# Optimization experiments

Measured on AMD Instinct MI355X. Metric: run time of the kernel, lower is better.

The kernel has to match this reference:

```python
import jax, jax.numpy as jnp
import numpy as np

IMG_SIZE = 224  # matches init_kwargs img_size


def setup_inputs() -> dict:
    key = jax.random.key(0)
    k1, k2, k3 = jax.random.split(key, 3)
    B, N = 128, 16384
    points = jax.random.uniform(k1, (B, N, 3), dtype=jnp.float32, minval=-1.0, maxval=1.0)
    azimuth = jax.random.uniform(k2, (B,), dtype=jnp.float32, minval=0.0, maxval=2.0 * np.pi)
    elevation = jax.random.uniform(k3, (B,), dtype=jnp.float32, minval=-0.5, maxval=0.5)
    return {"points": points, "azimuth": azimuth, "elevation": elevation}


def _rotation_matrices(azimuth, elevation):
    cა, sა = jnp.cos(azimuth), jnp.sin(azimuth)
    ce, se = jnp.cos(elevation), jnp.sin(elevation)
    z = jnp.zeros_like(cა)
    o = jnp.ones_like(cა)
    # R_az: rotation about y-axis, shape (B,3,3)
    R_az = jnp.stack([
        jnp.stack([cა, z, sა], -1),
        jnp.stack([z, o, z], -1),
        jnp.stack([-sა, z, cა], -1),
    ], axis=-2)
    # R_el: rotation about x-axis
    R_el = jnp.stack([
        jnp.stack([o, z, z], -1),
        jnp.stack([z, ce, -se], -1),
        jnp.stack([z, se, ce], -1),
    ], axis=-2)
    return jnp.einsum('bij,bjk->bik', R_el, R_az)


def reference(points, azimuth, elevation):
    B, N, _ = points.shape
    H = W = IMG_SIZE
    R = _rotation_matrices(azimuth, elevation)                 # (B,3,3)
    rotated = jnp.einsum('bni,bji->bnj', points, R)            # points @ R^T -> (B,N,3)

    points_2d = rotated[..., :2]
    z = rotated[..., 2]
    z_min = jnp.min(z, axis=1, keepdims=True)
    z_max = jnp.max(z, axis=1, keepdims=True)
    feat = 0.3 + 0.7 * (z - z_min) / (z_max - z_min + 1e-6)    # (B,N)

    px = (points_2d[..., 0] + 1.0) * 0.5 * W - 0.5
    py = (points_2d[..., 1] + 1.0) * 0.5 * H - 0.5
    px1 = jnp.floor(px); py1 = jnp.floor(py)
    px2 = px1 + 1.0;     py2 = py1 + 1.0

    w11 = (px2 - px) * (py2 - py)
    w12 = (px2 - px) * (py - py1)
    w21 = (px - px1) * (py2 - py)
    w22 = (px - px1) * (py - py1)

    mask = (px1 >= 0) & (py1 >= 0) & (px2 < W) & (py2 < H)     # (B,N)
    # fuse mask + feature into the weights instead of compacting (jit-friendly)
    vals = jnp.stack([w11, w12, w21, w22], axis=-1)            # (B,N,4)
    vals = vals * (feat * mask.astype(feat.dtype))[..., None]

    px1i = jnp.clip(px1, 0, W - 1).astype(jnp.int32)
    py1i = jnp.clip(py1, 0, H - 1).astype(jnp.int32)
    px2i = jnp.clip(px2, 0, W - 1).astype(jnp.int32)
    py2i = jnp.clip(py2, 0, H - 1).astype(jnp.int32)
    base = (jnp.arange(B, dtype=jnp.int32) * (H * W))[:, None]  # (B,1)
    idx = jnp.stack([
        base + py1i * W + px1i,
        base + py2i * W + px1i,
        base + py1i * W + px2i,
        base + py2i * W + px2i,
    ], axis=-1)                                                 # (B,N,4)

    image = jnp.zeros(B * H * W, dtype=vals.dtype)
    image = image.at[idx.reshape(-1)].add(vals.reshape(-1))
    image = image.reshape(B, 1, H, W)
    return jnp.broadcast_to(image, (B, 3, H, W))
```

## Files before the change

kernel.cpp:

```cpp
#include <hip/hip_runtime.h>

#define IMG 224
#define HW (IMG * IMG)
#define HW4 (HW / 4)
#define NB 128
#define NPTS 16384

#define QUARTERS 4
#define RPB (IMG / QUARTERS)
#define TILE_FLOATS (RPB * IMG)
#define THREADS 512

__global__ __launch_bounds__(THREADS) void k_render(const float* __restrict__ pts,
                                                    const float* __restrict__ az,
                                                    const float* __restrict__ el,
                                                    float* __restrict__ out) {
    const int b = blockIdx.x & (NB - 1);
    const int q = blockIdx.x >> 7;
    const int y0 = q * RPB;

    __shared__ float tile[TILE_FLOATS];
    __shared__ float wmin[THREADS / 64], wmax[THREADS / 64];

    float sa, ca, se, ce;
    __sincosf(az[b], &sa, &ca);
    __sincosf(el[b], &se, &ce);
    const float r00 = ca,       r02 = sa;
    const float r10 = se * sa,  r11 = ce,  r12 = -se * ca;
    const float r20 = -ce * sa, r21 = se,  r22 = ce * ca;

    for (int i = threadIdx.x; i < TILE_FLOATS; i += THREADS) tile[i] = 0.0f;

    const float4* __restrict__ pb4 = (const float4*)(pts + (size_t)b * NPTS * 3);

    float zmin = 1e30f, zmax = -1e30f;
    for (int it = 0; it < NPTS / (4 * THREADS); ++it) {
        const int t = it * THREADS + threadIdx.x;
        const float4 v0 = pb4[3 * t + 0];
        const float4 v1 = pb4[3 * t + 1];
        const float4 v2 = pb4[3 * t + 2];
        float rz;
        rz = r20 * v0.x + r21 * v0.y + r22 * v0.z; zmin = fminf(zmin, rz); zmax = fmaxf(zmax, rz);
        rz = r20 * v0.w + r21 * v1.x + r22 * v1.y; zmin = fminf(zmin, rz); zmax = fmaxf(zmax, rz);
        rz = r20 * v1.z + r21 * v1.w + r22 * v2.x; zmin = fminf(zmin, rz); zmax = fmaxf(zmax, rz);
        rz = r20 * v2.y + r21 * v2.z + r22 * v2.w; zmin = fminf(zmin, rz); zmax = fmaxf(zmax, rz);
    }
    for (int m = 1; m < 64; m <<= 1) {
        zmin = fminf(zmin, __shfl_xor(zmin, m));
        zmax = fmaxf(zmax, __shfl_xor(zmax, m));
    }
    const int wid = threadIdx.x >> 6;
    if ((threadIdx.x & 63) == 0) { wmin[wid] = zmin; wmax[wid] = zmax; }
    __syncthreads();
    zmin = wmin[0]; zmax = wmax[0];
#pragma unroll
    for (int w = 1; w < THREADS / 64; ++w) {
        zmin = fminf(zmin, wmin[w]);
        zmax = fmaxf(zmax, wmax[w]);
    }
    const float inv = 0.7f / (zmax - zmin + 1e-6f);

    auto splat = [&](float x, float y, float z) {
        const float rx = r00 * x + r02 * z;
        const float ry = r10 * x + r11 * y + r12 * z;
        const float rz = r20 * x + r21 * y + r22 * z;
        const float feat = 0.3f + (rz - zmin) * inv;

        const float px = (rx + 1.0f) * (0.5f * IMG) - 0.5f;
        const float py = (ry + 1.0f) * (0.5f * IMG) - 0.5f;
        const float px1 = floorf(px);
        const float py1 = floorf(py);
        if (px1 >= 0.0f && py1 >= 0.0f && px1 < (float)(IMG - 1) && py1 < (float)(IMG - 1)) {
            const float wx2 = px - px1;
            const float wx1 = 1.0f - wx2;
            const float wy2 = py - py1;
            const float wy1 = 1.0f - wy2;

            const int ix = (int)px1;
            const int iy = (int)py1;
            const int r0 = iy - y0;
            const int r1 = r0 + 1;
            if (r0 >= 0 && r0 < RPB) {
                atomicAdd(&tile[r0 * IMG + ix],     wx1 * wy1 * feat);
                atomicAdd(&tile[r0 * IMG + ix + 1], wx2 * wy1 * feat);
            }
            if (r1 >= 0 && r1 < RPB) {
                atomicAdd(&tile[r1 * IMG + ix],     wx1 * wy2 * feat);
                atomicAdd(&tile[r1 * IMG + ix + 1], wx2 * wy2 * feat);
            }
        }
    };

    for (int it = 0; it < NPTS / (4 * THREADS); ++it) {
        const int t = it * THREADS + threadIdx.x;
        const float4 v0 = pb4[3 * t + 0];
        const float4 v1 = pb4[3 * t + 1];
        const float4 v2 = pb4[3 * t + 2];
        splat(v0.x, v0.y, v0.z);
        splat(v0.w, v1.x, v1.y);
        splat(v1.z, v1.w, v2.x);
        splat(v2.y, v2.z, v2.w);
    }

    __syncthreads();

    const float4* __restrict__ t4 = (const float4*)tile;
    float4* __restrict__ o4 = (float4*)(out + (size_t)b * 3 * HW + (size_t)y0 * IMG);
    for (int i = threadIdx.x; i < TILE_FLOATS / 4; i += THREADS) {
        const float4 v = t4[i];
        o4[i] = v;
        o4[i + HW4] = v;
        o4[i + 2 * HW4] = v;
    }
}

extern "C" void kernel_launch(void* const* d_in, const int* in_sizes, int n_in,
                              void* d_out, int out_size, void* d_ws, size_t ws_size,
                              hipStream_t stream) {
    const float* pts = (const float*)d_in[0];
    const float* az  = (const float*)d_in[1];
    const float* el  = (const float*)d_in[2];
    float* out = (float*)d_out;

    k_render<<<NB * QUARTERS, THREADS, 0, stream>>>(pts, az, el, out);
}
```

Measured before the change: 133.5 us.

## Split image into eight row bands, unroll loops, use nontemporal output stores

Each image is now split across 8 blocks of 28 rows instead of 4 blocks of 56 rows, giving twice as many blocks and a smaller shared tile. The price is that every block re-reads all points of its image and recomputes the z min/max. The point loops are fully unrolled, the feature computation moves inside the in-bounds branch, and the output is written with nontemporal vector stores to avoid polluting the cache. More redundant global reads of the point cloud are the main risk.

```diff
diff --git a/kernel.cpp b/kernel.cpp
--- a/kernel.cpp
+++ b/kernel.cpp
@@ -6,21 +6,25 @@
 #define NB 128
 #define NPTS 16384
 
-#define QUARTERS 4
-#define RPB (IMG / QUARTERS)
-#define TILE_FLOATS (RPB * IMG)
+#define GROUPS 8
+#define RPB (IMG / GROUPS)
+#define TILEF (RPB * IMG)
 #define THREADS 512
+#define NW (THREADS / 64)
+
+typedef float vf4 __attribute__((ext_vector_type(4)));
 
 __global__ __launch_bounds__(THREADS) void k_render(const float* __restrict__ pts,
                                                     const float* __restrict__ az,
                                                     const float* __restrict__ el,
                                                     float* __restrict__ out) {
+    __shared__ __align__(16) float tile[TILEF];
+    __shared__ float wmin[NW], wmax[NW];
+
     const int b = blockIdx.x & (NB - 1);
-    const int q = blockIdx.x >> 7;
-    const int y0 = q * RPB;
-
-    __shared__ float tile[TILE_FLOATS];
-    __shared__ float wmin[THREADS / 64], wmax[THREADS / 64];
+    const int g = blockIdx.x >> 7;
+    const int y0 = g * RPB;
+    const int tid = threadIdx.x;
 
     float sa, ca, se, ce;
     __sincosf(az[b], &sa, &ca);
@@ -29,13 +33,14 @@
     const float r10 = se * sa,  r11 = ce,  r12 = -se * ca;
     const float r20 = -ce * sa, r21 = se,  r22 = ce * ca;
 
-    for (int i = threadIdx.x; i < TILE_FLOATS; i += THREADS) tile[i] = 0.0f;
-
     const float4* __restrict__ pb4 = (const float4*)(pts + (size_t)b * NPTS * 3);
 
+    for (int i = tid; i < TILEF; i += THREADS) tile[i] = 0.0f;
+
     float zmin = 1e30f, zmax = -1e30f;
+#pragma unroll
     for (int it = 0; it < NPTS / (4 * THREADS); ++it) {
-        const int t = it * THREADS + threadIdx.x;
+        const int t = it * THREADS + tid;
         const float4 v0 = pb4[3 * t + 0];
         const float4 v1 = pb4[3 * t + 1];
         const float4 v2 = pb4[3 * t + 2];
@@ -49,12 +54,10 @@
         zmin = fminf(zmin, __shfl_xor(zmin, m));
         zmax = fmaxf(zmax, __shfl_xor(zmax, m));
     }
-    const int wid = threadIdx.x >> 6;
-    if ((threadIdx.x & 63) == 0) { wmin[wid] = zmin; wmax[wid] = zmax; }
+    if ((tid & 63) == 0) { wmin[tid >> 6] = zmin; wmax[tid >> 6] = zmax; }
     __syncthreads();
-    zmin = wmin[0]; zmax = wmax[0];
 #pragma unroll
-    for (int w = 1; w < THREADS / 64; ++w) {
+    for (int w = 0; w < NW; ++w) {
         zmin = fminf(zmin, wmin[w]);
         zmax = fmaxf(zmax, wmax[w]);
     }
@@ -64,21 +67,16 @@
         const float rx = r00 * x + r02 * z;
         const float ry = r10 * x + r11 * y + r12 * z;
         const float rz = r20 * x + r21 * y + r22 * z;
-        const float feat = 0.3f + (rz - zmin) * inv;
-
         const float px = (rx + 1.0f) * (0.5f * IMG) - 0.5f;
         const float py = (ry + 1.0f) * (0.5f * IMG) - 0.5f;
-        const float px1 = floorf(px);
-        const float py1 = floorf(py);
-        if (px1 >= 0.0f && py1 >= 0.0f && px1 < (float)(IMG - 1) && py1 < (float)(IMG - 1)) {
-            const float wx2 = px - px1;
-            const float wx1 = 1.0f - wx2;
-            const float wy2 = py - py1;
-            const float wy1 = 1.0f - wy2;
-
-            const int ix = (int)px1;
-            const int iy = (int)py1;
-            const int r0 = iy - y0;
+        const float fx = floorf(px);
+        const float fy = floorf(py);
+        if (fx >= 0.0f && fy >= 0.0f && fx < (float)(IMG - 1) && fy < (float)(IMG - 1)) {
+            const float feat = 0.3f + (rz - zmin) * inv;
+            const float wx2 = px - fx, wx1 = 1.0f - wx2;
+            const float wy2 = py - fy, wy1 = 1.0f - wy2;
+            const int ix = (int)fx;
+            const int r0 = (int)fy - y0;
             const int r1 = r0 + 1;
             if (r0 >= 0 && r0 < RPB) {
                 atomicAdd(&tile[r0 * IMG + ix],     wx1 * wy1 * feat);
@@ -91,8 +89,9 @@
         }
     };
 
+#pragma unroll
     for (int it = 0; it < NPTS / (4 * THREADS); ++it) {
-        const int t = it * THREADS + threadIdx.x;
+        const int t = it * THREADS + tid;
         const float4 v0 = pb4[3 * t + 0];
         const float4 v1 = pb4[3 * t + 1];
         const float4 v2 = pb4[3 * t + 2];
@@ -104,13 +103,13 @@
 
     __syncthreads();
 
-    const float4* __restrict__ t4 = (const float4*)tile;
-    float4* __restrict__ o4 = (float4*)(out + (size_t)b * 3 * HW + (size_t)y0 * IMG);
-    for (int i = threadIdx.x; i < TILE_FLOATS / 4; i += THREADS) {
-        const float4 v = t4[i];
-        o4[i] = v;
-        o4[i + HW4] = v;
-        o4[i + 2 * HW4] = v;
+    const vf4* __restrict__ t4 = (const vf4*)tile;
+    vf4* __restrict__ o4 = (vf4*)(out + (size_t)b * 3 * HW + (size_t)y0 * IMG);
+    for (int i = tid; i < TILEF / 4; i += THREADS) {
+        const vf4 v = t4[i];
+        __builtin_nontemporal_store(v, o4 + i);
+        __builtin_nontemporal_store(v, o4 + i + HW4);
+        __builtin_nontemporal_store(v, o4 + i + 2 * HW4);
     }
 }
 
@@ -122,5 +121,5 @@
     const float* el  = (const float*)d_in[2];
     float* out = (float*)d_out;
 
-    k_render<<<NB * QUARTERS, THREADS, 0, stream>>>(pts, az, el, out);
+    k_render<<<NB * GROUPS, THREADS, 0, stream>>>(pts, az, el, out);
 }
```

Measured after the change: 138.6 us. +3.8%, slower.
